# Kernel tuning notes

Measured on AMD Instinct MI355X. Metric: run time of the kernel, lower is better.

Reference implementation:

```python
import jax, jax.numpy as jnp
import numpy as np

G = 8  # order of C8 rotation group

def expand_circulant(w):
    # w: [out_fields, in_fields, G] free params of a C8 regular->regular 1x1 conv.
    # Full weight: W[of*G+go, if*G+gi] = w[of, if, (go-gi) mod G]
    g = jnp.arange(G)
    idx = (g[:, None] - g[None, :]) % G            # [go, gi]
    Wf = w[:, :, idx]                              # [of, if, go, gi]
    Wf = jnp.transpose(Wf, (0, 2, 1, 3))           # [of, go, if, gi]
    return Wf.reshape(w.shape[0] * G, w.shape[1] * G)

def eq_proj(x2, w, b):
    # x2: [B, in_fields*G]; equivariant 1x1 conv = GEMM with circulant-expanded weight
    Wf = expand_circulant(w)                       # [out_fields*G, in_fields*G]
    bf = jnp.repeat(b, G)                          # per-field bias, shared across group dim
    return x2 @ Wf.T + bf

def setup_inputs() -> dict:
    key = jax.random.key(0)
    ks = jax.random.split(key, 12)
    B, d_model, n_head, d_k, d_v = 8192, 128, 8, 64, 64
    C = d_model * G                                # 1024
    s_in = 0.02
    inp = {
        'q': jax.random.normal(ks[0], (B, C, 1, 1), jnp.float32),
        'k': jax.random.normal(ks[1], (B, C, 1, 1), jnp.float32),
        'v': jax.random.normal(ks[2], (B, C, 1, 1), jnp.float32),
        'w_q': jax.random.normal(ks[3], (n_head * d_k, d_model, G), jnp.float32) * s_in,
        'b_q': jnp.zeros((n_head * d_k,), jnp.float32),
        'w_k': jax.random.normal(ks[4], (n_head * d_k, d_model, G), jnp.float32) * s_in,
        'b_k': jnp.zeros((n_head * d_k,), jnp.float32),
        'w_v': jax.random.normal(ks[5], (n_head * d_v, d_model, G), jnp.float32) * s_in,
        'b_v': jnp.zeros((n_head * d_v,), jnp.float32),
        'w_fc': jax.random.normal(ks[6], (d_model, n_head * d_v, G), jnp.float32) * s_in,
        'b_fc': jnp.zeros((d_model,), jnp.float32),
    }
    return inp

def reference(q, k, v, w_q, b_q, w_k, b_k, w_v, b_v, w_fc, b_fc):
    B, C = q.shape[0], q.shape[1]
    n_head, d_k = 8, 64
    d_v = 64
    temp = jnp.asarray(d_k ** 0.5, q.dtype)
    residual = q                                   # [B, C, 1, 1]
    q2 = q.reshape(B, C)
    k2 = k.reshape(B, C)
    v2 = v.reshape(B, C)
    # equivariant 1x1 conv projections -> [B, n_head*d_k*G]
    qp = eq_proj(q2, w_q, b_q).reshape(B, G, n_head, d_k).transpose(0, 2, 1, 3)  # [B,H,G,dk]
    kp = eq_proj(k2, w_k, b_k).reshape(B, G, n_head, d_k).transpose(0, 2, 1, 3)
    vp = eq_proj(v2, w_v, b_v).reshape(B, G, n_head, d_v).transpose(0, 2, 1, 3)
    # scaled dot-product attention over the G=8 group/orientation positions
    attn = jax.nn.softmax(jnp.einsum('bhqd,bhkd->bhqk', qp / temp, kp), axis=-1)  # [B,H,G,G]
    out = jnp.einsum('bhqk,bhkd->bhqd', attn, vp)  # [B,H,G,dv]
    # transpose(1,2) then flatten, exactly as torch .view(sz_b, -1, 1, 1)
    out = out.transpose(0, 2, 1, 3).reshape(B, G * n_head * d_v)
    out = eq_proj(out, w_fc, b_fc)                 # [B, d_model*G]
    out = out.reshape(B, C, 1, 1) + residual
    return out, attn
```

## Files before the change

### kernel.cpp

```cpp
#include <hip/hip_runtime.h>
#include <hip/hip_bf16.h>

typedef unsigned short u16;
typedef unsigned int u32;
typedef __bf16 bf16x8_t __attribute__((ext_vector_type(8)));
typedef float f32x4_t __attribute__((ext_vector_type(4)));

#define BK 64

__device__ __forceinline__ float b2f(u16 v) {
  return __uint_as_float(((u32)v) << 16);
}
__device__ __forceinline__ u16 f2b(float f) {
  __hip_bfloat16 h = __float2bfloat16(f);
  return *reinterpret_cast<u16*>(&h);
}
__device__ __forceinline__ float blo(u32 u) { return __uint_as_float(u << 16); }
__device__ __forceinline__ float bhi(u32 u) { return __uint_as_float(u & 0xffff0000u); }

__device__ __forceinline__ void async_lds16(const u16* g, u16* l) {
  __builtin_amdgcn_global_load_lds(
      (__attribute__((address_space(1))) void*)g,
      (__attribute__((address_space(3))) void*)l, 16, 0, 0);
}

__device__ __forceinline__ void expand8(const float* __restrict__ w,
                                        u16* __restrict__ dst, int I,
                                        int kshift, int gid) {
  const int n = gid >> kshift;
  const int kc = (gid & ((1 << kshift) - 1)) * 8;
  const int K = 8 << kshift;
  const float* wp = w + (size_t)((n >> 3) * I + (kc >> 3)) * 8;
  float4 w0 = *(const float4*)wp;
  float4 w1 = *(const float4*)(wp + 4);
  float w8[8] = {w0.x, w0.y, w0.z, w0.w, w1.x, w1.y, w1.z, w1.w};
  u16 t[8];
  const int r = (n - kc) & 7;
#pragma unroll
  for (int j = 0; j < 8; ++j) t[j] = f2b(w8[(r - j) & 7]);
  *(uint4*)(dst + (size_t)n * K + kc) = *(const uint4*)t;
}

__device__ __forceinline__ void cvt8(const float* __restrict__ src,
                                     u16* __restrict__ dst, int gid) {
  const float* p = src + (size_t)gid * 8;
  float4 a = *(const float4*)p;
  float4 b = *(const float4*)(p + 4);
  u16 t[8] = {f2b(a.x), f2b(a.y), f2b(a.z), f2b(a.w),
              f2b(b.x), f2b(b.y), f2b(b.z), f2b(b.w)};
  *(uint4*)(dst + (size_t)gid * 8) = *(const uint4*)t;
}

__global__ __launch_bounds__(256) void expand_all(
    const float* __restrict__ w_q, const float* __restrict__ w_k,
    const float* __restrict__ w_v, const float* __restrict__ w_fc,
    const float* __restrict__ q, const float* __restrict__ k,
    const float* __restrict__ v, u16* __restrict__ Wq, u16* __restrict__ Wk,
    u16* __restrict__ Wv, u16* __restrict__ Wfc, u16* __restrict__ qb,
    u16* __restrict__ kb, u16* __restrict__ vb, int cblocks) {
  const int e = blockIdx.x;
  if (e < 8192) {
    const int plane = e >> 11;
    const int gid = (e & 2047) * 256 + threadIdx.x;
    if (plane == 0) expand8(w_q, Wq, 128, 7, gid);
    else if (plane == 1) expand8(w_k, Wk, 128, 7, gid);
    else if (plane == 2) expand8(w_v, Wv, 128, 7, gid);
    else expand8(w_fc, Wfc, 512, 9, gid);
  } else {
    const int ce = e - 8192;
    const int plane = ce / cblocks;
    const int gid = (ce - plane * cblocks) * 256 + threadIdx.x;
    if (plane == 0) cvt8(q, qb, gid);
    else if (plane == 1) cvt8(k, kb, gid);
    else cvt8(v, vb, gid);
  }
}

__global__ __launch_bounds__(512, 2) void gemm_qkv8p(
    const u16* __restrict__ X0, const u16* __restrict__ X1,
    const u16* __restrict__ X2, const u16* __restrict__ W0,
    const u16* __restrict__ W1, const u16* __restrict__ W2,
    const float* __restrict__ b0v, const float* __restrict__ b1v,
    const float* __restrict__ b2v, u16* __restrict__ Y0, u16* __restrict__ Y1,
    u16* __restrict__ Y2, int M, int N, int K) {
  __shared__ __align__(16) u16 lds[65536];
  const int z = blockIdx.y;
  const u16* X = (z == 0) ? X0 : (z == 1) ? X1 : X2;
  const u16* W = (z == 0) ? W0 : (z == 1) ? W1 : W2;
  const float* bias = (z == 0) ? b0v : (z == 1) ? b1v : b2v;
  u16* Y = (z == 0) ? Y0 : (z == 1) ? Y1 : Y2;

  const int tid = threadIdx.x;
  const int bid = blockIdx.x;
  const int grid_m = M >> 8, grid_n = N >> 8;
  const int nb = grid_m * grid_n;
  int pid = (bid & 7) * (nb >> 3) + (bid >> 3);
  const int nig = 8 * grid_n;
  const int group_id = pid / nig;
  const int first_m = group_id * 8;
  const int gsz = min(8, grid_m - first_m);
  const int mt = first_m + (pid % gsz);
  const int ntile = (pid % nig) / gsz;
  const int m0 = mt << 8, n0 = ntile << 8;

  const int lane = tid & 63, wave = tid >> 6;
  const int wg = wave >> 2;
  const int wq = wave & 3;
  const int l16 = lane & 15, quad = lane >> 4;
  const int lswz = l16 & 7;

  const u16* gA = X + (size_t)m0 * K;
  const u16* gB = W + (size_t)n0 * K;
  const int srow = tid >> 3;
  const int skbg = (tid & 7) ^ (srow & 7);

  f32x4_t acc[8][4] = {};
  const int KT = K >> 6;
  const int niter = KT >> 1;

  auto stg = [&](int kt, int h, bool isB) {
    u16* l = lds + (isB ? 32768 : 0) + ((kt & 1) * 2 + h) * 8192 + tid * 8;
    const u16* g = (isB ? gB : gA) + (size_t)(h * 128 + srow) * K + kt * 64 +
                   skbg * 8;
    async_lds16(g, l);
    async_lds16(g + (size_t)64 * K, l + 4096);
  };
  auto ldA = [&](int kt, int mh, bf16x8_t (&a)[8]) {
    const u16* base = lds + ((kt & 1) * 2 + wg) * 8192 + (mh * 64 + l16) * 64;
#pragma unroll
    for (int mi = 0; mi < 4; ++mi)
#pragma unroll
      for (int ks = 0; ks < 2; ++ks)
        a[mi * 2 + ks] = *(const bf16x8_t*)(base + mi * 1024 +
                                            (((ks * 4 + quad) ^ lswz) * 8));
  };
  auto ldB = [&](int kt, int nh, bf16x8_t (&b)[4]) {
    const u16* base = lds + 32768 + ((kt & 1) * 2 + (wq >> 1)) * 8192 +
                      ((wq & 1) * 64 + nh * 32 + l16) * 64;
#pragma unroll
    for (int ni = 0; ni < 2; ++ni)
#pragma unroll
      for (int ks = 0; ks < 2; ++ks)
        b[ni * 2 + ks] = *(const bf16x8_t*)(base + ni * 1024 +
                                            (((ks * 4 + quad) ^ lswz) * 8));
  };
  auto mm = [&](int mh, int nh, bf16x8_t (&a)[8], bf16x8_t (&b)[4]) {
    __builtin_amdgcn_s_setprio(1);
#pragma unroll
    for (int mi = 0; mi < 4; ++mi)
#pragma unroll
      for (int ni = 0; ni < 2; ++ni)
#pragma unroll
        for (int ks = 0; ks < 2; ++ks)
          acc[mh * 4 + mi][nh * 2 + ni] = __builtin_amdgcn_mfma_f32_16x16x32_bf16(
              a[mi * 2 + ks], b[ni * 2 + ks], acc[mh * 4 + mi][nh * 2 + ni], 0,
              0, 0);
    __builtin_amdgcn_s_setprio(0);
  };
  auto bar = [] { __builtin_amdgcn_s_barrier(); };
  auto lgkm0 = [] {
    asm volatile("s_waitcnt lgkmcnt(0)" ::: "memory");
    __builtin_amdgcn_sched_barrier(0);
  };
  auto sched = [] { __builtin_amdgcn_sched_barrier(0); };

  bf16x8_t a0[8], a1[8], b0[4], b1[4];

  stg(0, 0, false); sched();
  stg(0, 0, true);  sched();
  stg(0, 1, false); sched();
  stg(0, 1, true);  sched();
  stg(1, 0, true);  sched();
  stg(1, 0, false); sched();
  asm volatile("s_waitcnt vmcnt(4)" ::: "memory");
  bar();
  sched();

  for (int it = 0; it < niter; ++it) {
    const int t = it * 2;
    const bool more = (t + 2 < KT);
    ldA(t, 0, a0); ldB(t, 0, b0);
    stg(t + 1, 1, false);
    sched(); bar(); lgkm0();
    mm(0, 0, a0, b0);
    bar();
    ldB(t, 1, b1);
    stg(t + 1, 1, true);
    sched(); bar(); lgkm0();
    mm(0, 1, a0, b1);
    bar();
    ldA(t, 1, a1);
    if (more) stg(t + 2, 0, true);
    sched(); bar(); lgkm0();
    mm(1, 1, a1, b1);
    bar();
    if (more) stg(t + 2, 0, false);
    sched();
    if (more) asm volatile("s_waitcnt vmcnt(4)" ::: "memory");
    else      asm volatile("s_waitcnt vmcnt(0)" ::: "memory");
    bar(); lgkm0();
    mm(1, 0, a1, b0);
    bar();
    ldA(t + 1, 0, a0); ldB(t + 1, 0, b0);
    if (more) stg(t + 2, 1, false);
    sched(); bar(); lgkm0();
    mm(0, 0, a0, b0);
    bar();
    ldB(t + 1, 1, b1);
    if (more) stg(t + 2, 1, true);
    sched(); bar(); lgkm0();
    mm(0, 1, a0, b1);
    bar();
    ldA(t + 1, 1, a1);
    if (more) stg(t + 3, 0, true);
    sched(); bar(); lgkm0();
    mm(1, 1, a1, b1);
    bar();
    if (more) {
      stg(t + 3, 0, false);
      sched();
      asm volatile("s_waitcnt vmcnt(4)" ::: "memory");
      bar(); lgkm0();
      mm(1, 0, a1, b0);
      bar();
    } else {
      lgkm0();
      mm(1, 0, a1, b0);
    }
  }

#pragma unroll
  for (int ni = 0; ni < 4; ++ni) {
    const int col = n0 + wq * 64 + ni * 16 + l16;
    const float bv = bias[col >> 3];
#pragma unroll
    for (int mi = 0; mi < 8; ++mi) {
#pragma unroll
      for (int r = 0; r < 4; ++r) {
        const int rw = m0 + wg * 128 + mi * 16 + quad * 4 + r;
        Y[(size_t)rw * N + col] = f2b(acc[mi][ni][r] + bv);
      }
    }
  }
}

template <int TN, bool HAS_RES, bool OUT_F32>
__device__ __forceinline__ void gemm_core(
    const u16* __restrict__ Xb, const u16* __restrict__ W,
    const float* __restrict__ bias, const float* __restrict__ res,
    void* __restrict__ Yv, int M, int N, int K, int bid) {
  __shared__ __align__(16) u16 As[128 * BK];
  __shared__ __align__(16) u16 Bs[TN * BK];
  const int tid = threadIdx.x;

  const int grid_m = M >> 7, grid_n = N / TN;
  const int nb = grid_m * grid_n;
  int pid = (bid & 7) * (nb >> 3) + (bid >> 3);
  const int nig = 8 * grid_n;
  const int group_id = pid / nig;
  const int first_m = group_id * 8;
  const int gsz = min(8, grid_m - first_m);
  const int mt = first_m + (pid % gsz);
  const int nt = (pid % nig) / gsz;
  const int m0 = mt << 7, n0 = nt * TN;

  const int lane = tid & 63;
  const int wave = tid >> 6;
  const int wm = (wave >> 1) * 64;
  const int wn = (wave & 1) * (TN / 2);
  const int l16 = lane & 15;
  const int quad = lane >> 4;
  constexpr int NJ = TN >> 5;

  f32x4_t acc[4][NJ] = {};

  const int row0 = tid >> 3;
  const int kgl = ((tid & 7) ^ (row0 & 7)) * 8;

  for (int k0 = 0; k0 < K; k0 += BK) {
#pragma unroll
    for (int it = 0; it < TN / 32; ++it)
      async_lds16(W + (size_t)(n0 + row0 + it * 32) * K + (k0 + kgl),
                  &Bs[(tid + it * 256) * 8]);
#pragma unroll
    for (int it = 0; it < 4; ++it)
      async_lds16(Xb + (size_t)(m0 + row0 + it * 32) * K + (k0 + kgl),
                  &As[(tid + it * 256) * 8]);
    __syncthreads();
#pragma unroll
    for (int half = 0; half < 2; ++half) {
      bf16x8_t af[4], bfr[NJ];
#pragma unroll
      for (int i = 0; i < 4; ++i)
        af[i] = *(const bf16x8_t*)&As[(wm + i * 16 + l16) * BK +
                                      (((quad + half * 4) ^ (l16 & 7)) * 8)];
#pragma unroll
      for (int j = 0; j < NJ; ++j)
        bfr[j] = *(const bf16x8_t*)&Bs[(wn + j * 16 + l16) * BK +
                                       (((quad + half * 4) ^ (l16 & 7)) * 8)];
#pragma unroll
      for (int i = 0; i < 4; ++i)
#pragma unroll
        for (int j = 0; j < NJ; ++j)
          acc[i][j] =
              __builtin_amdgcn_mfma_f32_16x16x32_bf16(af[i], bfr[j], acc[i][j], 0, 0, 0);
    }
    __syncthreads();
  }

#pragma unroll
  for (int j = 0; j < NJ; ++j) {
    const int col = n0 + wn + j * 16 + l16;
    const float bv = bias[col >> 3];
#pragma unroll
    for (int i = 0; i < 4; ++i) {
#pragma unroll
      for (int r = 0; r < 4; ++r) {
        const int rw = m0 + wm + i * 16 + quad * 4 + r;
        float vv = acc[i][j][r] + bv;
        if (HAS_RES) vv += res[(size_t)rw * N + col];
        if (OUT_F32)
          ((float*)Yv)[(size_t)rw * N + col] = vv;
        else
          ((u16*)Yv)[(size_t)rw * N + col] = f2b(vv);
      }
    }
  }
}

__global__ __launch_bounds__(256) void gemm_fc128(
    const u16* __restrict__ X, const u16* __restrict__ W,
    const float* __restrict__ bias, const float* __restrict__ res,
    float* __restrict__ Y, int M, int N, int K) {
  gemm_core<128, true, true>(X, W, bias, res, Y, M, N, K, blockIdx.x);
}
__global__ __launch_bounds__(256) void gemm_fc64(
    const u16* __restrict__ X, const u16* __restrict__ W,
    const float* __restrict__ bias, const float* __restrict__ res,
    float* __restrict__ Y, int M, int N, int K) {
  gemm_core<64, true, true>(X, W, bias, res, Y, M, N, K, blockIdx.x);
}

__global__ __launch_bounds__(256) void attn_kernel(
    const u16* qp, const u16* __restrict__ kp,
    const u16* __restrict__ vp, float* __restrict__ probs,
    u16* o, int iters) {
  __shared__ __align__(16) u16 Qs[4][8 * 72];
  __shared__ __align__(16) u16 Ks[4][8 * 72];
  __shared__ __align__(16) float Ps[4][64];
  const int tid = threadIdx.x;
  const int wave = tid >> 6;
  const int lane = tid & 63;
  const int r = lane >> 3, c = lane & 7;
  const int ls = r * 72 + c * 8;
  const int qg = r;
  const int kg = c;

  auto pairof = [&](int it) { return (it * gridDim.x + blockIdx.x) * 4 + wave; };
  auto gaddr = [&](int it) {
    const int pr = pairof(it);
    return (size_t)(pr >> 3) * 4096 + (size_t)r * 512 + (pr & 7) * 64 + c * 8;
  };

  uint4 qr = *(const uint4*)(qp + gaddr(0));
  uint4 kr = *(const uint4*)(kp + gaddr(0));

  for (int it = 0; it < iters; ++it) {
    *(uint4*)&Qs[wave][ls] = qr;
    *(uint4*)&Ks[wave][ls] = kr;
    const int pair = pairof(it);
    const int b = pair >> 3;
    const int h = pair & 7;
    float vcf[8];
#pragma unroll
    for (int k2 = 0; k2 < 8; ++k2)
      vcf[k2] = b2f(vp[(size_t)b * 4096 + (size_t)k2 * 512 + h * 64 + lane]);
    if (it + 1 < iters) {
      qr = *(const uint4*)(qp + gaddr(it + 1));
      kr = *(const uint4*)(kp + gaddr(it + 1));
    }
    float s = 0.f;
#pragma unroll
    for (int d8 = 0; d8 < 8; ++d8) {
      uint4 qa = *(const uint4*)&Qs[wave][qg * 72 + d8 * 8];
      uint4 ka = *(const uint4*)&Ks[wave][kg * 72 + d8 * 8];
      s += blo(qa.x) * blo(ka.x) + bhi(qa.x) * bhi(ka.x);
      s += blo(qa.y) * blo(ka.y) + bhi(qa.y) * bhi(ka.y);
      s += blo(qa.z) * blo(ka.z) + bhi(qa.z) * bhi(ka.z);
      s += blo(qa.w) * blo(ka.w) + bhi(qa.w) * bhi(ka.w);
    }
    s *= 0.125f;
    float mx = s;
    mx = fmaxf(mx, __shfl_xor(mx, 1));
    mx = fmaxf(mx, __shfl_xor(mx, 2));
    mx = fmaxf(mx, __shfl_xor(mx, 4));
    float e = __expf(s - mx);
    float sum = e;
    sum += __shfl_xor(sum, 1);
    sum += __shfl_xor(sum, 2);
    sum += __shfl_xor(sum, 4);
    const float p = e / sum;
    probs[(size_t)pair * 64 + lane] = p;
    Ps[wave][lane] = p;
#pragma unroll
    for (int q2 = 0; q2 < 8; ++q2) {
      float4 p0 = *(const float4*)&Ps[wave][q2 * 8];
      float4 p1 = *(const float4*)&Ps[wave][q2 * 8 + 4];
      float acc = p0.x * vcf[0] + p0.y * vcf[1] + p0.z * vcf[2] + p0.w * vcf[3] +
                  p1.x * vcf[4] + p1.y * vcf[5] + p1.z * vcf[6] + p1.w * vcf[7];
      o[(size_t)b * 4096 + q2 * 512 + h * 64 + lane] = f2b(acc);
    }
  }
}

extern "C" void kernel_launch(void* const* d_in, const int* in_sizes, int n_in,
                              void* d_out, int out_size, void* d_ws, size_t ws_size,
                              hipStream_t stream) {
  const float* q = (const float*)d_in[0];
  const float* k = (const float*)d_in[1];
  const float* v = (const float*)d_in[2];
  const float* w_q = (const float*)d_in[3];
  const float* b_q = (const float*)d_in[4];
  const float* w_k = (const float*)d_in[5];
  const float* b_k = (const float*)d_in[6];
  const float* w_v = (const float*)d_in[7];
  const float* b_v = (const float*)d_in[8];
  const float* w_fc = (const float*)d_in[9];
  const float* b_fc = (const float*)d_in[10];

  const int B = in_sizes[0] / 1024;
  float* out = (float*)d_out;
  float* probs = out + (size_t)B * 1024;

  u16* Wq = (u16*)d_ws;
  u16* Wk = Wq + (size_t)4096 * 1024;
  u16* Wv = Wk + (size_t)4096 * 1024;
  u16* Wfc = Wv + (size_t)4096 * 1024;
  u16* qb = Wfc + (size_t)4096 * 1024;
  u16* kb = qb + (size_t)B * 1024;
  u16* vb = kb + (size_t)B * 1024;
  u16* scratch = vb + (size_t)B * 1024;
  const size_t fixed_bytes =
      ((size_t)4 * 4096 * 1024 + (size_t)3 * B * 1024) * sizeof(u16);

  const size_t per_row = (size_t)(3 * 4096) * sizeof(u16);
  int chunkB = 256;
  for (int c = B; c >= 256; c >>= 1) {
    if (fixed_bytes + (size_t)c * per_row <= ws_size) { chunkB = c; break; }
  }

  u16* qp = scratch;
  u16* kp = qp + (size_t)chunkB * 4096;
  u16* vp = kp + (size_t)chunkB * 4096;
  u16* ao = qp;

  const int cblocks = B / 2;
  expand_all<<<8192 + 3 * cblocks, 256, 0, stream>>>(
      w_q, w_k, w_v, w_fc, q, k, v, Wq, Wk, Wv, Wfc, qb, kb, vb, cblocks);

  for (int cs = 0; cs < B; cs += chunkB) {
    const int nb_p = (chunkB / 256) * (4096 / 256);
    gemm_qkv8p<<<dim3(nb_p, 3), 512, 0, stream>>>(
        qb + (size_t)cs * 1024, kb + (size_t)cs * 1024, vb + (size_t)cs * 1024,
        Wq, Wk, Wv, b_q, b_k, b_v, qp, kp, vp, chunkB, 4096, 1024);
    const int ablocks = (chunkB >= 1024) ? 2048 : chunkB * 2;
    const int aiters = (chunkB * 8) / (ablocks * 4);
    attn_kernel<<<ablocks, 256, 0, stream>>>(qp, kp, vp,
                                             probs + (size_t)cs * 512, ao, aiters);
    if (chunkB >= 8192) {
      const int nb_fc = (chunkB / 128) * (1024 / 128);
      gemm_fc128<<<nb_fc, 256, 0, stream>>>(ao, Wfc, b_fc,
                                            q + (size_t)cs * 1024,
                                            out + (size_t)cs * 1024, chunkB,
                                            1024, 4096);
    } else {
      const int nb_fc = (chunkB / 128) * (1024 / 64);
      gemm_fc64<<<nb_fc, 256, 0, stream>>>(ao, Wfc, b_fc,
                                           q + (size_t)cs * 1024,
                                           out + (size_t)cs * 1024, chunkB,
                                           1024, 4096);
    }
  }
}
```

Before: 601.8 us.

## Vectorize QKV epilogue stores, stage V via LDS, and merge FC GEMM across chunks

The QKV GEMM epilogue now shuffles bf16 results between lanes so each lane writes four contiguous values as one 8-byte store instead of scattered 2-byte stores. The attention kernel loads V with 16-byte vector loads into LDS, prefetched one iteration ahead, instead of eight scalar loads. When the batch is split into two chunks, the attention outputs are kept in separate buffers and a single full-size FC GEMM with 128-wide tiles runs once at the end, replacing two half-size launches. This needs an extra scratch buffer per row, which may shrink the chosen chunk size when workspace is tight. The FC epilogue loop order is also swapped.

Result: faster. 570.2 us (-5.3%).

```diff
diff --git a/kernel.cpp b/kernel.cpp
--- a/kernel.cpp
+++ b/kernel.cpp
@@ -230,28 +230,53 @@
   }
 
 #pragma unroll
-  for (int ni = 0; ni < 4; ++ni) {
-    const int col = n0 + wq * 64 + ni * 16 + l16;
-    const float bv = bias[col >> 3];
-#pragma unroll
-    for (int mi = 0; mi < 8; ++mi) {
-#pragma unroll
-      for (int r = 0; r < 4; ++r) {
-        const int rw = m0 + wg * 128 + mi * 16 + quad * 4 + r;
-        Y[(size_t)rw * N + col] = f2b(acc[mi][ni][r] + bv);
+  for (int mi = 0; mi < 8; ++mi) {
+#pragma unroll
+    for (int r = 0; r < 4; ++r) {
+      const int rw = m0 + wg * 128 + mi * 16 + quad * 4 + r;
+      u32 h0, h1, h2, h3;
+      {
+        const int cb = n0 + wq * 64 + l16;
+        h0 = (u32)f2b(acc[mi][0][r] + bias[(cb) >> 3]);
+        h1 = (u32)f2b(acc[mi][1][r] + bias[(cb + 16) >> 3]);
+        h2 = (u32)f2b(acc[mi][2][r] + bias[(cb + 32) >> 3]);
+        h3 = (u32)f2b(acc[mi][3][r] + bias[(cb + 48) >> 3]);
       }
-    }
-  }
-}
-
-template <int TN, bool HAS_RES, bool OUT_F32>
-__device__ __forceinline__ void gemm_core(
-    const u16* __restrict__ Xb, const u16* __restrict__ W,
-    const float* __restrict__ bias, const float* __restrict__ res,
-    void* __restrict__ Yv, int M, int N, int K, int bid) {
+      const int s0 = quad * 16 + 4 * (l16 & 3);
+      u32 g0[4], g1[4], g2[4], g3[4];
+#pragma unroll
+      for (int j = 0; j < 4; ++j) {
+        g0[j] = (u32)__shfl((int)h0, s0 + j);
+        g1[j] = (u32)__shfl((int)h1, s0 + j);
+        g2[j] = (u32)__shfl((int)h2, s0 + j);
+        g3[j] = (u32)__shfl((int)h3, s0 + j);
+      }
+      const int myni = l16 >> 2;
+      u32 a_[4];
+#pragma unroll
+      for (int j = 0; j < 4; ++j) {
+        u32 s01 = (myni & 1) ? g1[j] : g0[j];
+        u32 s23 = (myni & 1) ? g3[j] : g2[j];
+        a_[j] = (myni & 2) ? s23 : s01;
+      }
+      uint2 wv;
+      wv.x = a_[0] | (a_[1] << 16);
+      wv.y = a_[2] | (a_[3] << 16);
+      *(uint2*)&Y[(size_t)rw * N + n0 + wq * 64 + 4 * l16] = wv;
+    }
+  }
+}
+
+__global__ __launch_bounds__(256) void gemm_fc2(
+    const u16* __restrict__ Aa, const u16* __restrict__ Ab,
+    const u16* __restrict__ W, const float* __restrict__ bias,
+    const float* __restrict__ res, float* __restrict__ Y, int M, int N, int K,
+    int halfM) {
+  constexpr int TN = 128;
   __shared__ __align__(16) u16 As[128 * BK];
   __shared__ __align__(16) u16 Bs[TN * BK];
   const int tid = threadIdx.x;
+  const int bid = blockIdx.x;
 
   const int grid_m = M >> 7, grid_n = N / TN;
   const int nb = grid_m * grid_n;
@@ -264,6 +289,9 @@
   const int nt = (pid % nig) / gsz;
   const int m0 = mt << 7, n0 = nt * TN;
 
+  const u16* Xb = (m0 < halfM) ? Aa : Ab;
+  const int m0l = (m0 < halfM) ? m0 : m0 - halfM;
+
   const int lane = tid & 63;
   const int wave = tid >> 6;
   const int wm = (wave >> 1) * 64;
@@ -284,7 +312,7 @@
                   &Bs[(tid + it * 256) * 8]);
 #pragma unroll
     for (int it = 0; it < 4; ++it)
-      async_lds16(Xb + (size_t)(m0 + row0 + it * 32) * K + (k0 + kgl),
+      async_lds16(Xb + (size_t)(m0l + row0 + it * 32) * K + (k0 + kgl),
                   &As[(tid + it * 256) * 8]);
     __syncthreads();
 #pragma unroll
@@ -309,44 +337,26 @@
   }
 
 #pragma unroll
-  for (int j = 0; j < NJ; ++j) {
-    const int col = n0 + wn + j * 16 + l16;
-    const float bv = bias[col >> 3];
-#pragma unroll
-    for (int i = 0; i < 4; ++i) {
-#pragma unroll
-      for (int r = 0; r < 4; ++r) {
-        const int rw = m0 + wm + i * 16 + quad * 4 + r;
-        float vv = acc[i][j][r] + bv;
-        if (HAS_RES) vv += res[(size_t)rw * N + col];
-        if (OUT_F32)
-          ((float*)Yv)[(size_t)rw * N + col] = vv;
-        else
-          ((u16*)Yv)[(size_t)rw * N + col] = f2b(vv);
+  for (int i = 0; i < 4; ++i) {
+#pragma unroll
+    for (int r = 0; r < 4; ++r) {
+      const int rw = m0 + wm + i * 16 + quad * 4 + r;
+#pragma unroll
+      for (int j = 0; j < NJ; ++j) {
+        const int col = n0 + wn + j * 16 + l16;
+        float vv = acc[i][j][r] + bias[col >> 3] + res[(size_t)rw * N + col];
+        Y[(size_t)rw * N + col] = vv;
       }
     }
   }
 }
 
-__global__ __launch_bounds__(256) void gemm_fc128(
-    const u16* __restrict__ X, const u16* __restrict__ W,
-    const float* __restrict__ bias, const float* __restrict__ res,
-    float* __restrict__ Y, int M, int N, int K) {
-  gemm_core<128, true, true>(X, W, bias, res, Y, M, N, K, blockIdx.x);
-}
-__global__ __launch_bounds__(256) void gemm_fc64(
-    const u16* __restrict__ X, const u16* __restrict__ W,
-    const float* __restrict__ bias, const float* __restrict__ res,
-    float* __restrict__ Y, int M, int N, int K) {
-  gemm_core<64, true, true>(X, W, bias, res, Y, M, N, K, blockIdx.x);
-}
-
 __global__ __launch_bounds__(256) void attn_kernel(
-    const u16* qp, const u16* __restrict__ kp,
-    const u16* __restrict__ vp, float* __restrict__ probs,
-    u16* o, int iters) {
+    const u16* __restrict__ qp, const u16* __restrict__ kp, const u16* vp,
+    float* __restrict__ probs, u16* o, int iters) {
   __shared__ __align__(16) u16 Qs[4][8 * 72];
   __shared__ __align__(16) u16 Ks[4][8 * 72];
+  __shared__ __align__(16) u16 Vs[4][512];
   __shared__ __align__(16) float Ps[4][64];
   const int tid = threadIdx.x;
   const int wave = tid >> 6;
@@ -361,23 +371,27 @@
     const int pr = pairof(it);
     return (size_t)(pr >> 3) * 4096 + (size_t)r * 512 + (pr & 7) * 64 + c * 8;
   };
+  auto vaddr = [&](int it) {
+    const int pr = pairof(it);
+    return (size_t)(pr >> 3) * 4096 + (size_t)(lane >> 3) * 512 +
+           (pr & 7) * 64 + (lane & 7) * 8;
+  };
 
   uint4 qr = *(const uint4*)(qp + gaddr(0));
   uint4 kr = *(const uint4*)(kp + gaddr(0));
+  uint4 vr = *(const uint4*)(vp + vaddr(0));
 
   for (int it = 0; it < iters; ++it) {
     *(uint4*)&Qs[wave][ls] = qr;
     *(uint4*)&Ks[wave][ls] = kr;
+    *(uint4*)&Vs[wave][lane * 8] = vr;
     const int pair = pairof(it);
     const int b = pair >> 3;
     const int h = pair & 7;
-    float vcf[8];
-#pragma unroll
-    for (int k2 = 0; k2 < 8; ++k2)
-      vcf[k2] = b2f(vp[(size_t)b * 4096 + (size_t)k2 * 512 + h * 64 + lane]);
     if (it + 1 < iters) {
       qr = *(const uint4*)(qp + gaddr(it + 1));
       kr = *(const uint4*)(kp + gaddr(it + 1));
+      vr = *(const uint4*)(vp + vaddr(it + 1));
     }
     float s = 0.f;
 #pragma unroll
@@ -402,6 +416,10 @@
     const float p = e / sum;
     probs[(size_t)pair * 64 + lane] = p;
     Ps[wave][lane] = p;
+    float vcf[8];
+#pragma unroll
+    for (int k2 = 0; k2 < 8; ++k2)
+      vcf[k2] = b2f(Vs[wave][k2 * 64 + lane]);
 #pragma unroll
     for (int q2 = 0; q2 < 8; ++q2) {
       float4 p0 = *(const float4*)&Ps[wave][q2 * 8];
@@ -443,7 +461,7 @@
   const size_t fixed_bytes =
       ((size_t)4 * 4096 * 1024 + (size_t)3 * B * 1024) * sizeof(u16);
 
-  const size_t per_row = (size_t)(3 * 4096) * sizeof(u16);
+  const size_t per_row = (size_t)(4 * 4096) * sizeof(u16);
   int chunkB = 256;
   for (int c = B; c >= 256; c >>= 1) {
     if (fixed_bytes + (size_t)c * per_row <= ws_size) { chunkB = c; break; }
@@ -452,12 +470,13 @@
   u16* qp = scratch;
   u16* kp = qp + (size_t)chunkB * 4096;
   u16* vp = kp + (size_t)chunkB * 4096;
-  u16* ao = qp;
+  u16* ao0 = vp + (size_t)chunkB * 4096;
 
   const int cblocks = B / 2;
   expand_all<<<8192 + 3 * cblocks, 256, 0, stream>>>(
       w_q, w_k, w_v, w_fc, q, k, v, Wq, Wk, Wv, Wfc, qb, kb, vb, cblocks);
 
+  const bool two_chunks = (chunkB * 2 == B);
   for (int cs = 0; cs < B; cs += chunkB) {
     const int nb_p = (chunkB / 256) * (4096 / 256);
     gemm_qkv8p<<<dim3(nb_p, 3), 512, 0, stream>>>(
@@ -465,20 +484,21 @@
         Wq, Wk, Wv, b_q, b_k, b_v, qp, kp, vp, chunkB, 4096, 1024);
     const int ablocks = (chunkB >= 1024) ? 2048 : chunkB * 2;
     const int aiters = (chunkB * 8) / (ablocks * 4);
+    u16* aoc = (cs == 0) ? ao0 : vp;
     attn_kernel<<<ablocks, 256, 0, stream>>>(qp, kp, vp,
-                                             probs + (size_t)cs * 512, ao, aiters);
-    if (chunkB >= 8192) {
+                                             probs + (size_t)cs * 512, aoc,
+                                             aiters);
+    if (!two_chunks) {
       const int nb_fc = (chunkB / 128) * (1024 / 128);
-      gemm_fc128<<<nb_fc, 256, 0, stream>>>(ao, Wfc, b_fc,
-                                            q + (size_t)cs * 1024,
-                                            out + (size_t)cs * 1024, chunkB,
-                                            1024, 4096);
-    } else {
-      const int nb_fc = (chunkB / 128) * (1024 / 64);
-      gemm_fc64<<<nb_fc, 256, 0, stream>>>(ao, Wfc, b_fc,
-                                           q + (size_t)cs * 1024,
-                                           out + (size_t)cs * 1024, chunkB,
-                                           1024, 4096);
-    }
-  }
-}
+      gemm_fc2<<<nb_fc, 256, 0, stream>>>(aoc, aoc, Wfc, b_fc,
+                                          q + (size_t)cs * 1024,
+                                          out + (size_t)cs * 1024, chunkB, 1024,
+                                          4096, chunkB);
+    }
+  }
+  if (two_chunks) {
+    const int nb_fc = (B / 128) * (1024 / 128);
+    gemm_fc2<<<nb_fc, 256, 0, stream>>>(ao0, vp, Wfc, b_fc, q, out, B, 1024,
+                                        4096, chunkB);
+  }
+}
```
